# Kernel optimization log

Measured on AMD Instinct MI355X. Metric: run time of the kernel, lower is better.

The kernel has to match this reference:

```python
import jax, jax.numpy as jnp
import numpy as np

N_WIRES = 8
DIM = 2 ** N_WIRES  # 256
NUM_HEADS = 4

def _cnot_ring_perm():
    # Compose CNOT(w, w+1) for w=0..6 then CNOT(7, 0) into one basis permutation.
    # Wire 0 is the most-significant bit of the basis index.
    perm = np.arange(DIM)
    pairs = [(w, w + 1) for w in range(N_WIRES - 1)] + [(N_WIRES - 1, 0)]
    j = np.arange(DIM)
    for c, t in pairs:
        ctrl = (j >> (N_WIRES - 1 - c)) & 1
        M = j ^ (ctrl << (N_WIRES - 1 - t))  # flip target bit where control=1 (involution)
        perm = perm[M]
    return perm

PERM = _cnot_ring_perm()
# SIGNS[i, w] = <i|Z_w|i> = 1 - 2*bit_w(i)
SIGNS = np.array([[1.0 - 2.0 * ((i >> (N_WIRES - 1 - w)) & 1) for w in range(N_WIRES)]
                  for i in range(DIM)], dtype=np.float32)

def setup_inputs() -> dict:
    key = jax.random.key(0)
    k1, k2, k3 = jax.random.split(key, 3)
    x = jax.random.normal(k1, (16, 4096, N_WIRES), jnp.float32)  # rotation angles per token
    theta = jax.random.normal(k2, (N_WIRES,), jnp.float32)       # trainable RX params
    w_combine = jax.random.normal(k3, (N_WIRES, N_WIRES), jnp.float32) / np.float32(np.sqrt(N_WIRES))
    b_combine = jnp.zeros((N_WIRES,), jnp.float32)
    return {"x": x, "theta": theta, "w_combine": w_combine, "b_combine": b_combine}

def _quantum_features(x, theta):
    # RX(x_i) then RX(theta_i) on wire i compose to RX(x_i + theta_i) acting on |0>.
    B, S, E = x.shape
    N = B * S
    phi = (x + theta).reshape(N, E)
    c = jnp.cos(0.5 * phi).astype(jnp.complex64)
    s = (-1j) * jnp.sin(0.5 * phi)          # RX|0> = cos(phi/2)|0> - i sin(phi/2)|1>
    wv = jnp.stack([c, s.astype(jnp.complex64)], axis=-1)  # (N, 8, 2)
    # Build product state via successive Kronecker products (wire 0 = MSB).
    state = jnp.ones((N, 1), jnp.complex64)
    for w in range(E):
        state = (state[:, :, None] * wv[:, w, None, :]).reshape(N, -1)  # (N, 2^(w+1))
    state = state[:, jnp.asarray(PERM)]      # apply the CNOT ring as one permutation
    probs = state.real ** 2 + state.imag ** 2  # (N, 256)
    return (probs @ jnp.asarray(SIGNS)).reshape(B, S, E)  # <Z_w> per token

def reference(x, theta, w_combine, b_combine):
    B, S, E = x.shape
    d_k = E // NUM_HEADS
    q = _quantum_features(x, theta)           # (B, S, 8); k = v = q in the source
    scores = jnp.einsum('bse,bte->bst', q, q) / np.float32(np.sqrt(d_k))
    attn = jax.nn.softmax(scores, axis=-1)    # dropout is identity in eval mode
    out = jnp.einsum('bst,bte->bse', attn, q)
    # Faithful to source: transpose(1,2).contiguous().view(B, S, E)
    out = jnp.swapaxes(out, 1, 2).reshape(B, S, E)
    return out @ w_combine.T + b_combine
```

## Files before the change

### kernel.cpp

```cpp
#include <hip/hip_runtime.h>
#include <math.h>


#define SEQ   4096
#define NB    16
#define TPB   256
#define SROWS 128
#define TC    512
#define NTILE (TC / 32)
#define KSTR  12

typedef _Float16 f16x2  __attribute__((ext_vector_type(2)));
typedef _Float16 f16x4  __attribute__((ext_vector_type(4)));
typedef float    f32x16 __attribute__((ext_vector_type(16)));

#if __has_builtin(__builtin_amdgcn_exp2f)
#define EXP2F(x) __builtin_amdgcn_exp2f(x)
#else
#define EXP2F(x) exp2f(x)
#endif

#if __has_builtin(__builtin_amdgcn_cvt_pkrtz)
#define PKRTZ(a, b) __builtin_amdgcn_cvt_pkrtz((a), (b))
#else
static __device__ __forceinline__ f16x2 PKRTZ(float a, float b) {
    return (f16x2){(_Float16)a, (_Float16)b};
}
#endif

__global__ __launch_bounds__(TPB, 4)
void qattn_kernel(const float* __restrict__ x, const float* __restrict__ theta,
                  const float* __restrict__ wc, const float* __restrict__ bc,
                  float* __restrict__ out)
{
    __shared__ __align__(16) _Float16 kf[TC * KSTR];
    __shared__ __align__(16) _Float16 vt[10 * 512];

    const int tid  = threadIdx.x;
    const int lane = tid & 63;
    const int wv   = tid >> 6;
    const int l31  = lane & 31;
    const int hp   = lane >> 5;

    const int b  = blockIdx.x >> 5;
    const int S0 = (blockIdx.x & 31) * SROWS;
    const float* xb = x + (size_t)b * SEQ * 8;

    float th[8];
#pragma unroll
    for (int w = 0; w < 8; ++w) th[w] = theta[w];

    f16x4 qfrag;
    {
        const int s = S0 + wv * 32 + l31;
        const float4 xa  = *(const float4*)(xb + s * 8);
        const float4 xb4 = *(const float4*)(xb + s * 8 + 4);
        float c0 = __cosf(xa.x  + th[0]);
        float c1 = __cosf(xa.y  + th[1]);
        float c2 = __cosf(xa.z  + th[2]);
        float c3 = __cosf(xa.w  + th[3]);
        float c4 = __cosf(xb4.x + th[4]);
        float c5 = __cosf(xb4.y + th[5]);
        float c6 = __cosf(xb4.z + th[6]);
        float c7 = __cosf(xb4.w + th[7]);
        float p1 = c0 * c1, p2 = p1 * c2, p3 = p2 * c3, p4 = p3 * c4;
        float p5 = p4 * c5, p6 = p5 * c6, p7 = p6 * c7;
        float p0 = c1 * c2 * c3 * c4 * c5 * c6 * c7;
        const float sc = 0.70710678118654752f * 1.44269504088896341f;
        if (hp == 0)
            qfrag = (f16x4){(_Float16)(p0*sc), (_Float16)(p1*sc),
                            (_Float16)(p2*sc), (_Float16)(p3*sc)};
        else
            qfrag = (f16x4){(_Float16)(p4*sc), (_Float16)(p5*sc),
                            (_Float16)(p6*sc), (_Float16)(p7*sc)};
    }

    f32x16 o = {0.f,0.f,0.f,0.f,0.f,0.f,0.f,0.f,0.f,0.f,0.f,0.f,0.f,0.f,0.f,0.f};

    const int wr = (l31 < 9) ? l31 : 9;
    const int vx = 2 * wr;
    const _Float16* kfb = kf + l31 * KSTR + 4 * hp;

    for (int ch = 0; ch < SEQ / TC; ++ch) {
        __syncthreads();
#pragma unroll
        for (int rr = 0; rr < TC / TPB; ++rr) {
            const int tt = rr * TPB + tid;
            const int t  = ch * TC + tt;
            const float4 xa  = *(const float4*)(xb + t * 8);
            const float4 xb4 = *(const float4*)(xb + t * 8 + 4);
            float c0 = __cosf(xa.x  + th[0]);
            float c1 = __cosf(xa.y  + th[1]);
            float c2 = __cosf(xa.z  + th[2]);
            float c3 = __cosf(xa.w  + th[3]);
            float c4 = __cosf(xb4.x + th[4]);
            float c5 = __cosf(xb4.y + th[5]);
            float c6 = __cosf(xb4.z + th[6]);
            float c7 = __cosf(xb4.w + th[7]);
            float p1 = c0 * c1, p2 = p1 * c2, p3 = p2 * c3, p4 = p3 * c4;
            float p5 = p4 * c5, p6 = p5 * c6, p7 = p6 * c7;
            float p0 = c1 * c2 * c3 * c4 * c5 * c6 * c7;
            _Float16 h0 = (_Float16)p0, h1 = (_Float16)p1, h2 = (_Float16)p2,
                     h3 = (_Float16)p3, h4 = (_Float16)p4, h5 = (_Float16)p5,
                     h6 = (_Float16)p6, h7 = (_Float16)p7;
            _Float16* krow = kf + tt * KSTR;
            *(f16x4*)(krow)     = (f16x4){h0, h1, h2, h3};
            *(f16x4*)(krow + 4) = (f16x4){h4, h5, h6, h7};
            const int c  = tt >> 1;
            const int hb = tt & 1;
            vt[2*(0*256 + (c ^  0)) + hb] = h0;
            vt[2*(1*256 + (c ^  2)) + hb] = h1;
            vt[2*(2*256 + (c ^  4)) + hb] = h2;
            vt[2*(3*256 + (c ^  6)) + hb] = h3;
            vt[2*(4*256 + (c ^  8)) + hb] = h4;
            vt[2*(5*256 + (c ^ 10)) + hb] = h5;
            vt[2*(6*256 + (c ^ 12)) + hb] = h6;
            vt[2*(7*256 + (c ^ 14)) + hb] = h7;
            vt[2*(8*256 + (c ^ 16)) + hb] = (_Float16)1.0f;
        }
        __syncthreads();
#pragma unroll 2
        for (int i = 0; i < NTILE; ++i) {
            f16x4 kfrag = *(const f16x4*)(kfb + i * 32 * KSTR);
            f32x16 cc = __builtin_amdgcn_mfma_f32_32x32x8f16(
                kfrag, qfrag, (f32x16){0.f,0.f,0.f,0.f,0.f,0.f,0.f,0.f,
                                       0.f,0.f,0.f,0.f,0.f,0.f,0.f,0.f}, 0, 0, 0);
#pragma unroll
            for (int u = 0; u < 4; ++u) {
                auto lo = PKRTZ(EXP2F(cc[4*u+0]), EXP2F(cc[4*u+1]));
                auto hi = PKRTZ(EXP2F(cc[4*u+2]), EXP2F(cc[4*u+3]));
                f16x4 pf;
                pf.x = lo.x; pf.y = lo.y; pf.z = hi.x; pf.w = hi.y;
                const int cw   = 16*i + 4*u + 2*hp;
                const int phys = wr * 256 + (cw ^ vx);
                f16x4 vfrag = *(const f16x4*)(vt + 2 * phys);
                o = __builtin_amdgcn_mfma_f32_32x32x8f16(pf, vfrag, o, 0, 0, 0);
            }
        }
    }

    float dd[16];
    const int src = (lane & 32) | 8;
#pragma unroll
    for (int r = 0; r < 16; ++r) dd[r] = __shfl(o[r], src, 64);

    __syncthreads();
    float* attn = (float*)kf;
    if (l31 < 8) {
#pragma unroll
        for (int r = 0; r < 16; ++r) {
            const int sloc = wv * 32 + (r & 3) + 8 * (r >> 2) + 4 * hp;
            attn[sloc * 9 + l31] = o[r] / dd[r];
        }
    }
    __syncthreads();

    if (tid < 128) {
        const int e    = tid >> 4;
        const int nloc = tid & 15;
        const int r    = e * 512 + (S0 >> 3) + nloc;
        float y[8];
#pragma unroll
        for (int c = 0; c < 8; ++c) y[c] = attn[(nloc * 8 + c) * 9 + e];
        float oo[8];
#pragma unroll
        for (int k = 0; k < 8; ++k) {
            float a = bc[k];
#pragma unroll
            for (int c = 0; c < 8; ++c) a += y[c] * wc[k * 8 + c];
            oo[k] = a;
        }
        float4* op = (float4*)(out + ((size_t)b * SEQ + r) * 8);
        op[0] = make_float4(oo[0], oo[1], oo[2], oo[3]);
        op[1] = make_float4(oo[4], oo[5], oo[6], oo[7]);
    }
}

extern "C" void kernel_launch(void* const* d_in, const int* in_sizes, int n_in,
                              void* d_out, int out_size, void* d_ws, size_t ws_size,
                              hipStream_t stream)
{
    const float* x  = (const float*)d_in[0];
    const float* th = (const float*)d_in[1];
    const float* wc = (const float*)d_in[2];
    const float* bc = (const float*)d_in[3];
    float* out = (float*)d_out;

    qattn_kernel<<<dim3(NB * (SEQ / SROWS)), dim3(TPB), 0, stream>>>(x, th, wc, bc, out);
}
```

Baseline: 109.0 us.

## Split key dimension across four wave groups per block with LDS reduction

Grows the block from 256 to 1024 threads. Four groups of four waves each handle a quarter of every 1024-key chunk for the same 128 query rows, so one thread now builds each key row in LDS. Each group's partial numerator and denominator accumulators go to LDS, are summed across groups, and normalised before the output projection. The aim is to put far more waves on each CU and hide MFMA/exp latency. The cost is an extra LDS reduction pass with additional barriers.

```diff
diff --git a/kernel.cpp b/kernel.cpp
--- a/kernel.cpp
+++ b/kernel.cpp
@@ -4,13 +4,13 @@
 
 #define SEQ   4096
 #define NB    16
-#define TPB   256
 #define SROWS 128
-#define TC    512
-#define NTILE (TC / 32)
+#define TPB   1024
+#define NTG   4
+#define TC    1024
+#define TILES_PER_TG 8
 #define KSTR  12
 
-typedef _Float16 f16x2  __attribute__((ext_vector_type(2)));
 typedef _Float16 f16x4  __attribute__((ext_vector_type(4)));
 typedef float    f32x16 __attribute__((ext_vector_type(16)));
 
@@ -20,25 +20,21 @@
 #define EXP2F(x) exp2f(x)
 #endif
 
-#if __has_builtin(__builtin_amdgcn_cvt_pkrtz)
-#define PKRTZ(a, b) __builtin_amdgcn_cvt_pkrtz((a), (b))
-#else
-static __device__ __forceinline__ f16x2 PKRTZ(float a, float b) {
-    return (f16x2){(_Float16)a, (_Float16)b};
-}
-#endif
-
-__global__ __launch_bounds__(TPB, 4)
+__global__ __launch_bounds__(TPB, 8)
 void qattn_kernel(const float* __restrict__ x, const float* __restrict__ theta,
                   const float* __restrict__ wc, const float* __restrict__ bc,
                   float* __restrict__ out)
 {
     __shared__ __align__(16) _Float16 kf[TC * KSTR];
-    __shared__ __align__(16) _Float16 vt[10 * 512];
+    __shared__ __align__(16) _Float16 vt[10 * TC];
+    float* part = (float*)kf;
+    float* attn = (float*)vt;
 
     const int tid  = threadIdx.x;
     const int lane = tid & 63;
     const int wv   = tid >> 6;
+    const int sub  = wv & 3;
+    const int tg   = wv >> 2;
     const int l31  = lane & 31;
     const int hp   = lane >> 5;
 
@@ -52,7 +48,7 @@
 
     f16x4 qfrag;
     {
-        const int s = S0 + wv * 32 + l31;
+        const int s = S0 + sub * 32 + l31;
         const float4 xa  = *(const float4*)(xb + s * 8);
         const float4 xb4 = *(const float4*)(xb + s * 8 + 4);
         float c0 = __cosf(xa.x  + th[0]);
@@ -79,13 +75,12 @@
 
     const int wr = (l31 < 9) ? l31 : 9;
     const int vx = 2 * wr;
-    const _Float16* kfb = kf + l31 * KSTR + 4 * hp;
+    const _Float16* kfb = kf + l31 * KSTR + 4 * hp + (tg * TILES_PER_TG) * 32 * KSTR;
 
     for (int ch = 0; ch < SEQ / TC; ++ch) {
         __syncthreads();
-#pragma unroll
-        for (int rr = 0; rr < TC / TPB; ++rr) {
-            const int tt = rr * TPB + tid;
+        {
+            const int tt = tid;
             const int t  = ch * TC + tt;
             const float4 xa  = *(const float4*)(xb + t * 8);
             const float4 xb4 = *(const float4*)(xb + t * 8 + 4);
@@ -108,54 +103,63 @@
             *(f16x4*)(krow + 4) = (f16x4){h4, h5, h6, h7};
             const int c  = tt >> 1;
             const int hb = tt & 1;
-            vt[2*(0*256 + (c ^  0)) + hb] = h0;
-            vt[2*(1*256 + (c ^  2)) + hb] = h1;
-            vt[2*(2*256 + (c ^  4)) + hb] = h2;
-            vt[2*(3*256 + (c ^  6)) + hb] = h3;
-            vt[2*(4*256 + (c ^  8)) + hb] = h4;
-            vt[2*(5*256 + (c ^ 10)) + hb] = h5;
-            vt[2*(6*256 + (c ^ 12)) + hb] = h6;
-            vt[2*(7*256 + (c ^ 14)) + hb] = h7;
-            vt[2*(8*256 + (c ^ 16)) + hb] = (_Float16)1.0f;
+            vt[2*(0*512 + (c ^  0)) + hb] = h0;
+            vt[2*(1*512 + (c ^  2)) + hb] = h1;
+            vt[2*(2*512 + (c ^  4)) + hb] = h2;
+            vt[2*(3*512 + (c ^  6)) + hb] = h3;
+            vt[2*(4*512 + (c ^  8)) + hb] = h4;
+            vt[2*(5*512 + (c ^ 10)) + hb] = h5;
+            vt[2*(6*512 + (c ^ 12)) + hb] = h6;
+            vt[2*(7*512 + (c ^ 14)) + hb] = h7;
+            vt[2*(8*512 + (c ^ 16)) + hb] = (_Float16)1.0f;
         }
         __syncthreads();
 #pragma unroll 2
-        for (int i = 0; i < NTILE; ++i) {
+        for (int i = 0; i < TILES_PER_TG; ++i) {
             f16x4 kfrag = *(const f16x4*)(kfb + i * 32 * KSTR);
             f32x16 cc = __builtin_amdgcn_mfma_f32_32x32x8f16(
                 kfrag, qfrag, (f32x16){0.f,0.f,0.f,0.f,0.f,0.f,0.f,0.f,
                                        0.f,0.f,0.f,0.f,0.f,0.f,0.f,0.f}, 0, 0, 0);
 #pragma unroll
             for (int u = 0; u < 4; ++u) {
-                auto lo = PKRTZ(EXP2F(cc[4*u+0]), EXP2F(cc[4*u+1]));
-                auto hi = PKRTZ(EXP2F(cc[4*u+2]), EXP2F(cc[4*u+3]));
+                auto lo = __builtin_amdgcn_cvt_pkrtz(EXP2F(cc[4*u+0]), EXP2F(cc[4*u+1]));
+                auto hi = __builtin_amdgcn_cvt_pkrtz(EXP2F(cc[4*u+2]), EXP2F(cc[4*u+3]));
                 f16x4 pf;
                 pf.x = lo.x; pf.y = lo.y; pf.z = hi.x; pf.w = hi.y;
-                const int cw   = 16*i + 4*u + 2*hp;
-                const int phys = wr * 256 + (cw ^ vx);
+                const int cw   = 16 * (tg * TILES_PER_TG + i) + 4*u + 2*hp;
+                const int phys = wr * 512 + (cw ^ vx);
                 f16x4 vfrag = *(const f16x4*)(vt + 2 * phys);
                 o = __builtin_amdgcn_mfma_f32_32x32x8f16(pf, vfrag, o, 0, 0, 0);
             }
         }
     }
 
-    float dd[16];
-    const int src = (lane & 32) | 8;
-#pragma unroll
-    for (int r = 0; r < 16; ++r) dd[r] = __shfl(o[r], src, 64);
-
     __syncthreads();
-    float* attn = (float*)kf;
-    if (l31 < 8) {
+    if (l31 < 9) {
 #pragma unroll
         for (int r = 0; r < 16; ++r) {
-            const int sloc = wv * 32 + (r & 3) + 8 * (r >> 2) + 4 * hp;
-            attn[sloc * 9 + l31] = o[r] / dd[r];
+            const int sloc = sub * 32 + (r & 3) + 8 * (r >> 2) + 4 * hp;
+            part[((tg * SROWS) + sloc) * 9 + l31] = o[r];
         }
     }
     __syncthreads();
+    for (int idx = tid; idx < SROWS * 9; idx += TPB) {
+        const int rr = idx / 9;
+        const int w  = idx - rr * 9;
+        float sm = 0.f;
+#pragma unroll
+        for (int g = 0; g < NTG; ++g) sm += part[((g * SROWS) + rr) * 9 + w];
+        attn[rr * 9 + w] = sm;
+    }
+    __syncthreads();
+    if (tid < SROWS * 8) {
+        const int rr = tid >> 3;
+        const int w  = tid & 7;
+        attn[rr * 9 + w] = attn[rr * 9 + w] / attn[rr * 9 + 8];
+    }
+    __syncthreads();
 
-    if (tid < 128) {
+    if (tid < SROWS) {
         const int e    = tid >> 4;
         const int nloc = tid & 15;
         const int r    = e * 512 + (S0 >> 3) + nloc;
```

New measurement: 96.40 us. 11.6% less time.
